# Performance work log

Hardware: AMD Instinct MI355X
Metric: run time of the kernel (lower is better)

The kernel has to match this reference:

```python
import jax, jax.numpy as jnp
import numpy as np

KS = 17  # structuring element size
R = KS // 2  # radius 8


def _ellipse_kernel():
    # replicates cv2.getStructuringElement(cv2.MORPH_ELLIPSE, (17, 17)):
    # per row dy, fill columns within dx = round(sqrt(r^2 - dy^2))
    k = np.zeros((KS, KS), np.float32)
    for i in range(KS):
        dy = i - R
        dx = int(round(np.sqrt(max(0.0, float(R * R - dy * dy)))))
        k[i, R - dx:R + dx + 1] = 1.0
    return k


def _morph(v, kern, erode):
    # exact TF min-plus erosion2d / max-plus dilation2d with SAME padding
    # (pad +inf for erosion, -inf for dilation), filters = kern per channel.
    B, H, W, C = v.shape
    pad_val = np.inf if erode else -np.inf
    sgn = -1.0 if erode else 1.0
    red = jnp.min if erode else jnp.max
    comb = jnp.minimum if erode else jnp.maximum
    vp = jnp.pad(v, ((0, 0), (0, 0), (R, R), (0, 0)), constant_values=pad_val)
    X = jnp.stack([vp[:, :, k:k + W, :] for k in range(KS)], axis=0)
    # per kernel row dy: 1D min/max-plus correlation along x
    rows = [red(X + sgn * kern[dy][:, None, None, None, None], axis=0) for dy in range(KS)]
    Rst = jnp.pad(jnp.stack(rows, axis=0), ((0, 0), (0, 0), (R, R), (0, 0), (0, 0)), constant_values=pad_val)
    out = Rst[0][:, 0:H]
    for dy in range(1, KS):
        out = comb(out, Rst[dy][:, dy:dy + H])
    return out


def _mask_edges(masks, kern):
    # flip border rows/cols (corners flipped twice -> original)
    m = jnp.concatenate([1.0 - masks[:, :1], masks[:, 1:-1], 1.0 - masks[:, -1:]], axis=1)
    m = jnp.concatenate([1.0 - m[:, :, :1], m[:, :, 1:-1], 1.0 - m[:, :, -1:]], axis=2)
    eroded = _morph(m, kern, erode=True) + 1.0
    dilated = _morph(m, kern, erode=False) - 1.0
    return dilated - eroded


def setup_inputs() -> dict:
    key = jax.random.key(0)
    k1, k2, k3 = jax.random.split(key, 3)
    B, H, W, C = 8, 512, 512, 3
    in_detections = jax.random.randint(k1, (B, H, W, C), 0, 2).astype(jnp.float32)
    p_detections = jax.random.normal(k2, (B, H, W, C), dtype=jnp.float32)
    edge_weight = 1.0 + 39.0 * jax.random.uniform(k3, (1, 1, 1, C), dtype=jnp.float32)
    in_masks = jnp.ones((B, C), dtype=jnp.float32)
    logvars = -3.0 * jnp.ones((1, C), dtype=jnp.float32)
    return {"in_masks": in_masks, "in_detections": in_detections,
            "p_detections": p_detections, "edge_weight": edge_weight,
            "logvars": logvars}


def reference(in_masks, in_detections, p_detections, edge_weight, logvars):
    kern = jnp.asarray(_ellipse_kernel())
    edges = _mask_edges(in_detections, kern)  # (B,H,W,C)
    weights = 1.0 + (edge_weight - 1.0) * edges
    weights = weights / jnp.sum(weights, axis=(1, 2), keepdims=True)
    pix = jnp.where(in_detections == 1.0,
                    jnp.maximum(0.0, 1.0 - p_detections) ** 2,
                    jnp.maximum(0.0, p_detections) ** 2)
    raw = jnp.sum(weights * pix, axis=(1, 2))  # (B,C)
    losses = jnp.exp(-logvars) * raw + logvars  # (B,C)
    return jnp.mean(in_masks * losses, axis=1)  # (B,)
```

## Files before the change

kernel.cpp:

```cpp
#include <hip/hip_runtime.h>
#include <stdint.h>


#define TILE 16
#define NT   32
#define MAGIC64 0x7F3B9E1DC0FFEE42ull

__global__ __launch_bounds__(1024) void k_fused(const float* __restrict__ det,
                                                const float* __restrict__ pdet,
                                                float* partials,
                                                unsigned long long* tags,
                                                const float* __restrict__ in_masks,
                                                const float* __restrict__ ew,
                                                const float* __restrict__ lv,
                                                float* __restrict__ out) {
  __shared__ uint64_t mb[3][32][9];
  __shared__ uint64_t pl2[2][32][90];
  __shared__ uint64_t eg[3][TILE][8];
  __shared__ float red[16][6];
  __shared__ int cw[3][2];
  __shared__ float term[8][3];

  int blk = blockIdx.x;
  int b = blk & 7;
  int tile = blk >> 3;
  int r0 = tile * TILE;
  int tid = threadIdx.x;
  int wv = tid >> 6, lane = tid & 63;

  float dv[8][3], pv[8][3];
#pragma unroll
  for (int it = 0; it < 8; ++it) {
    int task = wv * 8 + it;
    int rl = task >> 3, w = task & 7;
    size_t base = (((((size_t)b << 9) + (r0 + rl)) << 9) + (w << 6) + lane) * 3;
    dv[it][0] = det[base];
    dv[it][1] = det[base + 1];
    dv[it][2] = det[base + 2];
  }
#pragma unroll
  for (int it = 0; it < 8; ++it) {
    int task = wv * 8 + it;
    int rl = task >> 3, w = task & 7;
    size_t base = (((((size_t)b << 9) + (r0 + rl)) << 9) + (w << 6) + lane) * 3;
    pv[it][0] = pdet[base];
    pv[it][1] = pdet[base + 1];
    pv[it][2] = pdet[base + 2];
  }
#pragma unroll
  for (int it = 0; it < 8; ++it) {
    int task = wv * 8 + it;
    int rl = task >> 3, w = task & 7;
    uint64_t b0 = __ballot(dv[it][0] == 1.0f);
    uint64_t b1 = __ballot(dv[it][1] == 1.0f);
    uint64_t b2 = __ballot(dv[it][2] == 1.0f);
    if (lane == 0) { mb[0][rl + 8][w] = b0; mb[1][rl + 8][w] = b1; mb[2][rl + 8][w] = b2; }
  }
#pragma unroll
  for (int it = 0; it < 8; ++it) {
    int task = wv * 8 + it;
    int rlh = task >> 3, w = task & 7;
    int grow = (rlh < 8) ? (r0 - 8 + rlh) : (r0 + 8 + rlh);
    int mrow = (rlh < 8) ? rlh : (16 + rlh);
    float h0 = 0.f, h1 = 0.f, h2 = 0.f;
    if (grow >= 0 && grow < 512) {
      size_t base = (((((size_t)b << 9) + grow) << 9) + (w << 6) + lane) * 3;
      h0 = det[base]; h1 = det[base + 1]; h2 = det[base + 2];
    }
    uint64_t b0 = __ballot(h0 == 1.0f);
    uint64_t b1 = __ballot(h1 == 1.0f);
    uint64_t b2 = __ballot(h2 == 1.0f);
    if (lane == 0) { mb[0][mrow][w] = b0; mb[1][mrow][w] = b1; mb[2][mrow][w] = b2; }
  }
  __syncthreads();

  const int PD[9] = {5, 5, 5, 4, 4, 3, 2, 1, 0};

  {
    int ch = tid >> 9;
    int t5 = tid & 511;
    int side = t5 >> 8;
    int t2 = t5 & 255;
    int rl = t2 >> 3, w = t2 & 7;
    int grow = r0 - 8 + rl;
    bool valid = (grow >= 0 && grow < 512);
    uint64_t x = 0, xl = 0, xh = 0;
    if (valid) {
      x = mb[ch][rl][w];
      xl = (w > 0) ? mb[ch][rl][w - 1] : 0;
      xh = (w < 7) ? mb[ch][rl][w + 1] : 0;
      if (grow == 0 || grow == 511) {
        x = ~x; xl = (w > 0) ? ~xl : 0; xh = (w < 7) ? ~xh : 0;
      }
      if (w == 0) x ^= 1ull;
      if (w == 7) x ^= (1ull << 63);
      if (side) {
        x = ~x; xl = (w > 0) ? ~xl : 0; xh = (w < 7) ? ~xh : 0;
      }
    }
    uint64_t* P = &pl2[ch][rl][0];
    if (!side) P[w] = x;
    uint64_t d = x;
#pragma unroll
    for (int s = 1; s <= 8; ++s) {
      d |= (x << s) | (xl >> (64 - s)) | (x >> s) | (xh << (64 - s));
      if (s >= 4) P[(s - 3 + side * 5) * 8 + w] = d;
    }
  }
  __syncthreads();

  if (tid < 256) {
    int ch = tid >> 7;
    int t3 = tid & 127;
    int rl = t3 >> 3, w = t3 & 7;
    uint64_t dil = 0, erc = 0;
#pragma unroll
    for (int dy = -8; dy <= 8; ++dy) {
      int ady = dy < 0 ? -dy : dy;
      int pr = rl + 8 + dy;
      if (ady == 8) {
        int grow = r0 - 8 + pr;
        uint64_t m = pl2[ch][pr][w];
        dil |= m;
        erc |= (grow >= 0 && grow < 512) ? ~m : 0;
      } else {
        dil |= pl2[ch][pr][PD[ady] * 8 + w];
        erc |= pl2[ch][pr][(PD[ady] + 5) * 8 + w];
      }
    }
    uint64_t e = dil & erc;
    eg[ch][rl][w] = e;
    int c = __popcll(e);
#pragma unroll
    for (int off = 32; off >= 1; off >>= 1) c += __shfl_xor(c, off);
    if (lane == 0) cw[ch][(tid >> 6) & 1] = c;
  }
  __syncthreads();

  if (tid < 512) {
    int side = tid >> 8;
    int t2 = tid & 255;
    int rl = t2 >> 3, w = t2 & 7;
    int grow = r0 - 8 + rl;
    bool valid = (grow >= 0 && grow < 512);
    uint64_t x = 0, xl = 0, xh = 0;
    if (valid) {
      x = mb[2][rl][w];
      xl = (w > 0) ? mb[2][rl][w - 1] : 0;
      xh = (w < 7) ? mb[2][rl][w + 1] : 0;
      if (grow == 0 || grow == 511) {
        x = ~x; xl = (w > 0) ? ~xl : 0; xh = (w < 7) ? ~xh : 0;
      }
      if (w == 0) x ^= 1ull;
      if (w == 7) x ^= (1ull << 63);
      if (side) {
        x = ~x; xl = (w > 0) ? ~xl : 0; xh = (w < 7) ? ~xh : 0;
      }
    }
    uint64_t* P = &pl2[0][rl][0];
    if (!side) P[w] = x;
    uint64_t d = x;
#pragma unroll
    for (int s = 1; s <= 8; ++s) {
      d |= (x << s) | (xl >> (64 - s)) | (x >> s) | (xh << (64 - s));
      if (s >= 4) P[(s - 3 + side * 5) * 8 + w] = d;
    }
  }
  __syncthreads();

  if (tid < 128) {
    int rl = tid >> 3, w = tid & 7;
    uint64_t dil = 0, erc = 0;
#pragma unroll
    for (int dy = -8; dy <= 8; ++dy) {
      int ady = dy < 0 ? -dy : dy;
      int pr = rl + 8 + dy;
      if (ady == 8) {
        int grow = r0 - 8 + pr;
        uint64_t m = pl2[0][pr][w];
        dil |= m;
        erc |= (grow >= 0 && grow < 512) ? ~m : 0;
      } else {
        dil |= pl2[0][pr][PD[ady] * 8 + w];
        erc |= pl2[0][pr][(PD[ady] + 5) * 8 + w];
      }
    }
    uint64_t e = dil & erc;
    eg[2][rl][w] = e;
    int c = __popcll(e);
#pragma unroll
    for (int off = 32; off >= 1; off >>= 1) c += __shfl_xor(c, off);
    if (lane == 0) cw[2][wv] = c;
  }
  __syncthreads();

  float sA0 = 0, sA1 = 0, sA2 = 0, sE0 = 0, sE1 = 0, sE2 = 0;
#pragma unroll
  for (int it = 0; it < 8; ++it) {
    int task = wv * 8 + it;
    int rl = task >> 3, w = task & 7;
    float p0 = pv[it][0], p1 = pv[it][1], p2 = pv[it][2];
    uint64_t E0 = eg[0][rl][w], E1 = eg[1][rl][w], E2 = eg[2][rl][w];
    float v0 = (dv[it][0] == 1.0f) ? 1.0f - p0 : p0; v0 = fmaxf(v0, 0.f); v0 *= v0;
    float v1 = (dv[it][1] == 1.0f) ? 1.0f - p1 : p1; v1 = fmaxf(v1, 0.f); v1 *= v1;
    float v2 = (dv[it][2] == 1.0f) ? 1.0f - p2 : p2; v2 = fmaxf(v2, 0.f); v2 *= v2;
    sA0 += v0; sA1 += v1; sA2 += v2;
    if ((E0 >> lane) & 1) sE0 += v0;
    if ((E1 >> lane) & 1) sE1 += v1;
    if ((E2 >> lane) & 1) sE2 += v2;
  }
#pragma unroll
  for (int off = 32; off >= 1; off >>= 1) {
    sA0 += __shfl_xor(sA0, off); sA1 += __shfl_xor(sA1, off); sA2 += __shfl_xor(sA2, off);
    sE0 += __shfl_xor(sE0, off); sE1 += __shfl_xor(sE1, off); sE2 += __shfl_xor(sE2, off);
  }
  if (lane == 0) {
    red[wv][0] = sA0; red[wv][1] = sA1; red[wv][2] = sA2;
    red[wv][3] = sE0; red[wv][4] = sE1; red[wv][5] = sE2;
  }
  __syncthreads();

  if (tid < 6) {
    float s = 0.f;
    for (int i = 0; i < 16; ++i) s += red[i][tid];
    __hip_atomic_store(&partials[blk * 9 + tid], s,
                       __ATOMIC_RELAXED, __HIP_MEMORY_SCOPE_AGENT);
  } else if (tid < 9) {
    int chx = tid - 6;
    __hip_atomic_store(&partials[blk * 9 + tid], (float)(cw[chx][0] + cw[chx][1]),
                       __ATOMIC_RELAXED, __HIP_MEMORY_SCOPE_AGENT);
  }
  __syncthreads();
  if (tid == 0)
    __hip_atomic_store(&tags[blk], MAGIC64,
                       __ATOMIC_RELEASE, __HIP_MEMORY_SCOPE_AGENT);

  if (blk != 0) return;
  if (tid < 256) {
    while (__hip_atomic_load(&tags[tid], __ATOMIC_ACQUIRE,
                             __HIP_MEMORY_SCOPE_AGENT) != MAGIC64)
      __builtin_amdgcn_s_sleep(8);
  }
  __syncthreads();

  if (tid < 24) {
    int b8 = tid / 3, ch = tid - 3 * b8;
    float sA = 0.f, sE = 0.f, cn = 0.f;
    for (int t = 0; t < NT; ++t) {
      float* P = partials + (size_t)((t << 3) | b8) * 9;
      sA += __hip_atomic_load(&P[ch], __ATOMIC_RELAXED, __HIP_MEMORY_SCOPE_AGENT);
      sE += __hip_atomic_load(&P[3 + ch], __ATOMIC_RELAXED, __HIP_MEMORY_SCOPE_AGENT);
      cn += __hip_atomic_load(&P[6 + ch], __ATOMIC_RELAXED, __HIP_MEMORY_SCOPE_AGENT);
    }
    float w1 = ew[ch] - 1.0f;
    float S = 262144.0f + w1 * cn;
    float raw = (sA + w1 * sE) / S;
    term[b8][ch] = in_masks[b8 * 3 + ch] * (expf(-lv[ch]) * raw + lv[ch]);
  }
  __syncthreads();
  if (tid < 8) out[tid] = (term[tid][0] + term[tid][1] + term[tid][2]) * (1.0f / 3.0f);
}

extern "C" void kernel_launch(void* const* d_in, const int* in_sizes, int n_in,
                              void* d_out, int out_size, void* d_ws, size_t ws_size,
                              hipStream_t stream) {
  const float* in_masks = (const float*)d_in[0];
  const float* det = (const float*)d_in[1];
  const float* pdet = (const float*)d_in[2];
  const float* ew = (const float*)d_in[3];
  const float* lv = (const float*)d_in[4];
  float* out = (float*)d_out;

  float* partials = (float*)d_ws;
  unsigned long long* tags =
      (unsigned long long*)(partials + 256 * 9);

  k_fused<<<256, 1024, 0, stream>>>(det, pdet, partials, tags,
                                    in_masks, ew, lv, out);
}
```

Measured before the change: 23.68 us.

## Process all three channels' morphology in one pass and defer pdet loads

Expands the shared bitmask plane buffer to hold all three channels (moved to dynamic LDS, about 69 KB), so the horizontal-dilation and vertical-combine phases for every channel run in a single pass. This removes two barrier-separated phases where channel 2 was handled alone by a subset of threads. The p_detections loads are moved after the first barrier, which lowers register pressure during the det loads. The cost is higher LDS use per block and an extra hipFuncSetAttribute call on every launch.

```diff
diff --git a/kernel.cpp b/kernel.cpp
--- a/kernel.cpp
+++ b/kernel.cpp
@@ -5,6 +5,7 @@
 #define TILE 16
 #define NT   32
 #define MAGIC64 0x7F3B9E1DC0FFEE42ull
+#define PL(ch, pr) (pl_dyn + ((size_t)((ch) * 32 + (pr))) * 90)
 
 __global__ __launch_bounds__(1024) void k_fused(const float* __restrict__ det,
                                                 const float* __restrict__ pdet,
@@ -14,8 +15,8 @@
                                                 const float* __restrict__ ew,
                                                 const float* __restrict__ lv,
                                                 float* __restrict__ out) {
+  extern __shared__ uint64_t pl_dyn[];
   __shared__ uint64_t mb[3][32][9];
-  __shared__ uint64_t pl2[2][32][90];
   __shared__ uint64_t eg[3][TILE][8];
   __shared__ float red[16][6];
   __shared__ int cw[3][2];
@@ -28,7 +29,7 @@
   int tid = threadIdx.x;
   int wv = tid >> 6, lane = tid & 63;
 
-  float dv[8][3], pv[8][3];
+  float dv[8][3];
 #pragma unroll
   for (int it = 0; it < 8; ++it) {
     int task = wv * 8 + it;
@@ -37,15 +38,6 @@
     dv[it][0] = det[base];
     dv[it][1] = det[base + 1];
     dv[it][2] = det[base + 2];
-  }
-#pragma unroll
-  for (int it = 0; it < 8; ++it) {
-    int task = wv * 8 + it;
-    int rl = task >> 3, w = task & 7;
-    size_t base = (((((size_t)b << 9) + (r0 + rl)) << 9) + (w << 6) + lane) * 3;
-    pv[it][0] = pdet[base];
-    pv[it][1] = pdet[base + 1];
-    pv[it][2] = pdet[base + 2];
   }
 #pragma unroll
   for (int it = 0; it < 8; ++it) {
@@ -74,14 +66,18 @@
   }
   __syncthreads();
 
-  const int PD[9] = {5, 5, 5, 4, 4, 3, 2, 1, 0};
-
-  {
-    int ch = tid >> 9;
-    int t5 = tid & 511;
-    int side = t5 >> 8;
-    int t2 = t5 & 255;
-    int rl = t2 >> 3, w = t2 & 7;
+  float pv[8][3];
+#pragma unroll
+  for (int it = 0; it < 8; ++it) {
+    int task = wv * 8 + it;
+    int rl = task >> 3, w = task & 7;
+    size_t base = (((((size_t)b << 9) + (r0 + rl)) << 9) + (w << 6) + lane) * 3;
+    pv[it][0] = pdet[base];
+    pv[it][1] = pdet[base + 1];
+    pv[it][2] = pdet[base + 2];
+  }
+
+  auto hchain = [&](int ch, int side, int rl, int w) {
     int grow = r0 - 8 + rl;
     bool valid = (grow >= 0 && grow < 512);
     uint64_t x = 0, xl = 0, xh = 0;
@@ -98,7 +94,7 @@
         x = ~x; xl = (w > 0) ? ~xl : 0; xh = (w < 7) ? ~xh : 0;
       }
     }
-    uint64_t* P = &pl2[ch][rl][0];
+    uint64_t* P = PL(ch, rl);
     if (!side) P[w] = x;
     uint64_t d = x;
 #pragma unroll
@@ -106,10 +102,16 @@
       d |= (x << s) | (xl >> (64 - s)) | (x >> s) | (xh << (64 - s));
       if (s >= 4) P[(s - 3 + side * 5) * 8 + w] = d;
     }
-  }
-  __syncthreads();
-
-  if (tid < 256) {
+  };
+  {
+    hchain(tid >> 9, (tid >> 8) & 1, (tid >> 3) & 31, tid & 7);
+    if (tid < 512) hchain(2, tid >> 8, (tid >> 3) & 31, tid & 7);
+  }
+  __syncthreads();
+
+  const int PD[9] = {5, 5, 5, 4, 4, 3, 2, 1, 0};
+
+  if (tid < 384) {
     int ch = tid >> 7;
     int t3 = tid & 127;
     int rl = t3 >> 3, w = t3 & 7;
@@ -120,12 +122,12 @@
       int pr = rl + 8 + dy;
       if (ady == 8) {
         int grow = r0 - 8 + pr;
-        uint64_t m = pl2[ch][pr][w];
+        uint64_t m = PL(ch, pr)[w];
         dil |= m;
         erc |= (grow >= 0 && grow < 512) ? ~m : 0;
       } else {
-        dil |= pl2[ch][pr][PD[ady] * 8 + w];
-        erc |= pl2[ch][pr][(PD[ady] + 5) * 8 + w];
+        dil |= PL(ch, pr)[PD[ady] * 8 + w];
+        erc |= PL(ch, pr)[(PD[ady] + 5) * 8 + w];
       }
     }
     uint64_t e = dil & erc;
@@ -134,63 +136,6 @@
 #pragma unroll
     for (int off = 32; off >= 1; off >>= 1) c += __shfl_xor(c, off);
     if (lane == 0) cw[ch][(tid >> 6) & 1] = c;
-  }
-  __syncthreads();
-
-  if (tid < 512) {
-    int side = tid >> 8;
-    int t2 = tid & 255;
-    int rl = t2 >> 3, w = t2 & 7;
-    int grow = r0 - 8 + rl;
-    bool valid = (grow >= 0 && grow < 512);
-    uint64_t x = 0, xl = 0, xh = 0;
-    if (valid) {
-      x = mb[2][rl][w];
-      xl = (w > 0) ? mb[2][rl][w - 1] : 0;
-      xh = (w < 7) ? mb[2][rl][w + 1] : 0;
-      if (grow == 0 || grow == 511) {
-        x = ~x; xl = (w > 0) ? ~xl : 0; xh = (w < 7) ? ~xh : 0;
-      }
-      if (w == 0) x ^= 1ull;
-      if (w == 7) x ^= (1ull << 63);
-      if (side) {
-        x = ~x; xl = (w > 0) ? ~xl : 0; xh = (w < 7) ? ~xh : 0;
-      }
-    }
-    uint64_t* P = &pl2[0][rl][0];
-    if (!side) P[w] = x;
-    uint64_t d = x;
-#pragma unroll
-    for (int s = 1; s <= 8; ++s) {
-      d |= (x << s) | (xl >> (64 - s)) | (x >> s) | (xh << (64 - s));
-      if (s >= 4) P[(s - 3 + side * 5) * 8 + w] = d;
-    }
-  }
-  __syncthreads();
-
-  if (tid < 128) {
-    int rl = tid >> 3, w = tid & 7;
-    uint64_t dil = 0, erc = 0;
-#pragma unroll
-    for (int dy = -8; dy <= 8; ++dy) {
-      int ady = dy < 0 ? -dy : dy;
-      int pr = rl + 8 + dy;
-      if (ady == 8) {
-        int grow = r0 - 8 + pr;
-        uint64_t m = pl2[0][pr][w];
-        dil |= m;
-        erc |= (grow >= 0 && grow < 512) ? ~m : 0;
-      } else {
-        dil |= pl2[0][pr][PD[ady] * 8 + w];
-        erc |= pl2[0][pr][(PD[ady] + 5) * 8 + w];
-      }
-    }
-    uint64_t e = dil & erc;
-    eg[2][rl][w] = e;
-    int c = __popcll(e);
-#pragma unroll
-    for (int off = 32; off >= 1; off >>= 1) c += __shfl_xor(c, off);
-    if (lane == 0) cw[2][wv] = c;
   }
   __syncthreads();
 
@@ -275,6 +220,10 @@
   unsigned long long* tags =
       (unsigned long long*)(partials + 256 * 9);
 
-  k_fused<<<256, 1024, 0, stream>>>(det, pdet, partials, tags,
-                                    in_masks, ew, lv, out);
+  const int dyn_lds = 3 * 32 * 90 * (int)sizeof(uint64_t);
+  (void)hipFuncSetAttribute((const void*)k_fused,
+                            hipFuncAttributeMaxDynamicSharedMemorySize, dyn_lds);
+
+  k_fused<<<256, 1024, dyn_lds, stream>>>(det, pdet, partials, tags,
+                                          in_masks, ew, lv, out);
 }
```

New measurement: 20.01 us (median of 2 runs). 1.18x faster.
